# Kernel tuning notes

Hardware: AMD Instinct MI355X
Metric: run time of the kernel (lower is better)

The kernel has to match this reference:

```python
import jax, jax.numpy as jnp
import numpy as np

K, d = 8, 8
D = K * d          # 64
B, T, N = 8, 12, 325


def _xavier(key, shape):
    fan_out, fan_in = shape
    lim = (6.0 / (fan_in + fan_out)) ** 0.5
    return jax.random.uniform(key, shape, jnp.float32, -lim, lim)


def setup_inputs() -> dict:
    key = jax.random.key(0)
    ks = jax.random.split(key, 8)
    return {
        "X": jax.random.normal(ks[0], (B, T, N, D), jnp.float32),
        "STE": jax.random.normal(ks[1], (B, T, N, D), jnp.float32),
        "adj": jax.random.randint(ks[2], (N, N), 0, 2, jnp.int32),
        "W7": _xavier(ks[3], (D, 2 * D)), "b7": jnp.zeros((D,), jnp.float32),
        "W8": _xavier(ks[4], (D, 2 * D)), "b8": jnp.zeros((D,), jnp.float32),
        "W9": _xavier(ks[5], (D, 2 * D)), "b9": jnp.zeros((D,), jnp.float32),
        "W10": _xavier(ks[6], (D, D)), "b10": jnp.zeros((D,), jnp.float32),
        "W11": _xavier(ks[7], (D, D)), "b11": jnp.zeros((D,), jnp.float32),
    }


def reference(X, STE, adj, W7, b7, W8, b8, W9, b9, W10, b10, W11, b11):
    # X, STE: [B, T, N, D]
    x = jnp.concatenate([X, STE], axis=-1)  # [B,T,N,2D]
    gelu = lambda t: jax.nn.gelu(t, approximate=False)  # torch F.gelu default = exact erf
    q = gelu(x @ W7.T + b7)  # [B,T,N,D]
    k = gelu(x @ W8.T + b8)
    v = gelu(x @ W9.T + b9)
    # split D into K heads of size d (equivalent to torch split(dim=-1)+cat(dim=0))
    heads = lambda t: t.reshape(B, T, N, K, d)
    q, k, v = heads(q), heads(k), heads(v)
    # scores: [K,B,T,N,N] == torch's [K*B,T,N,N]
    attn = jnp.einsum('btnkd,btmkd->kbtnm', q, k) / (d ** 0.5)
    attn = jnp.where(adj > 0, attn, jnp.float32(-9e15))
    attn = jax.nn.softmax(attn, axis=-1)
    out = jnp.einsum('kbtnm,btmkd->btnkd', attn, v).reshape(B, T, N, D)
    out = gelu(out @ W10.T + b10) @ W11.T + b11
    return out
```

## Files before the change

kernel.cpp:

```cpp
#include <hip/hip_runtime.h>
#include <math.h>

#define NN 325
#define BT 96
#define NROWS (BT * NN)
#define SCL (0.35355339059327373f * 1.4426950408889634f)

typedef _Float16 half_t;
typedef half_t half4_t __attribute__((ext_vector_type(4)));
typedef half_t half2_t __attribute__((ext_vector_type(2)));
typedef float float4_t __attribute__((ext_vector_type(4)));

__device__ __forceinline__ float gelu_f(float x) {
    return 0.5f * x * (1.0f + erff(x * 0.70710678118654752f));
}

__global__ void pack_adj_kernel(const int* __restrict__ adj,
                                unsigned int* __restrict__ packedT)
{
    int idx = blockIdx.x * 256 + threadIdx.x;
    if (idx >= 11 * NN) return;
    int w = idx / NN, n = idx - w * NN;
    unsigned int bits = 0u;
    #pragma unroll 8
    for (int j = 0; j < 32; ++j) {
        int m = w * 32 + j;
        if (m < NN && adj[n * NN + m] > 0) bits |= (1u << j);
    }
    packedT[w * NN + n] = bits;
}

#define XS 136

__device__ __forceinline__ void qkv_mfma_phase(
    const half_t* x16, const half_t* w16p, const float* __restrict__ b,
    half_t* __restrict__ outp, float oscale,
    int row0, int rbase, int l15, int quad)
{
    float4_t acc[4];
    #pragma unroll
    for (int ct = 0; ct < 4; ++ct) {
        float bias = b[ct * 16 + l15];
        acc[ct] = (float4_t){bias, bias, bias, bias};
    }
    #pragma unroll
    for (int kk = 0; kk < 8; ++kk) {
        half4_t a = *(const half4_t*)&x16[(rbase + l15) * XS + kk * 16 + quad * 4];
        #pragma unroll
        for (int ct = 0; ct < 4; ++ct) {
            half4_t bf = *(const half4_t*)&w16p[(ct * 16 + l15) * XS + kk * 16 + quad * 4];
            acc[ct] = __builtin_amdgcn_mfma_f32_16x16x16f16(a, bf, acc[ct], 0, 0, 0);
        }
    }
    #pragma unroll
    for (int ct = 0; ct < 4; ++ct) {
        #pragma unroll
        for (int rr = 0; rr < 4; ++rr) {
            int R = row0 + rbase + quad * 4 + rr;
            if (R < NROWS)
                outp[R * 64 + ct * 16 + l15] =
                    (half_t)(gelu_f(acc[ct][rr]) * oscale);
        }
    }
}

__global__ __launch_bounds__(256) void qkv_kernel(
    const float* __restrict__ X, const float* __restrict__ STE,
    const float* __restrict__ W7, const float* __restrict__ b7,
    const float* __restrict__ W8, const float* __restrict__ b8,
    const float* __restrict__ W9, const float* __restrict__ b9,
    half_t* __restrict__ q, half_t* __restrict__ k, half_t* __restrict__ v)
{
    __shared__ __attribute__((aligned(16))) half_t x16[64 * XS];
    __shared__ __attribute__((aligned(16))) half_t w16[3][64 * XS];
    const int tid  = threadIdx.x;
    const int row0 = blockIdx.x * 64;

    #pragma unroll 2
    for (int idx = tid; idx < 64 * 32; idx += 256) {
        int r = idx >> 5, c4 = idx & 31;
        int R = row0 + r;
        float4 f = {0.f, 0.f, 0.f, 0.f};
        if (R < NROWS)
            f = (c4 < 16) ? *(const float4*)(X + R * 64 + c4 * 4)
                          : *(const float4*)(STE + R * 64 + (c4 - 16) * 4);
        half4_t hv;
        hv[0] = (half_t)f.x; hv[1] = (half_t)f.y;
        hv[2] = (half_t)f.z; hv[3] = (half_t)f.w;
        *(half4_t*)&x16[r * XS + c4 * 4] = hv;
    }
    #pragma unroll 2
    for (int idx = tid; idx < 3 * 64 * 32; idx += 256) {
        int p = idx >> 11, rem = idx & 2047;
        int c = rem >> 5, c4 = rem & 31;
        const float* Wp = (p == 0) ? W7 : (p == 1) ? W8 : W9;
        float4 f = *(const float4*)(Wp + c * 128 + c4 * 4);
        half4_t hv;
        hv[0] = (half_t)f.x; hv[1] = (half_t)f.y;
        hv[2] = (half_t)f.z; hv[3] = (half_t)f.w;
        *(half4_t*)&w16[p][c * XS + c4 * 4] = hv;
    }
    __syncthreads();

    const int lane = tid & 63, wv = tid >> 6;
    const int l15 = lane & 15, quad = lane >> 4;
    const int rbase = wv * 16;

    qkv_mfma_phase(x16, w16[0], b7, q, SCL, row0, rbase, l15, quad);
    qkv_mfma_phase(x16, w16[1], b8, k, 1.0f, row0, rbase, l15, quad);
    qkv_mfma_phase(x16, w16[2], b9, v, 1.0f, row0, rbase, l15, quad);
}

__global__ __launch_bounds__(256) void attn_kernel(
    const half_t* __restrict__ q16g, const half_t* __restrict__ k16g,
    const half_t* __restrict__ v16g, const unsigned int* __restrict__ packedT,
    half_t* __restrict__ ao)
{
    __shared__ __attribute__((aligned(16))) half_t Q16[336 * 20];
    __shared__ __attribute__((aligned(16))) half_t K16[336 * 20];
    __shared__ __attribute__((aligned(16))) half_t VT16[16 * 344];
    const int tid = threadIdx.x;
    const int h = blockIdx.x, bt = blockIdx.y;
    const long base = (long)(bt * NN) * 64 + h * 8;

    const half4_t z4 = {(half_t)0.f, (half_t)0.f, (half_t)0.f, (half_t)0.f};

    for (int r = tid; r < 336; r += 256) {
        half4_t qa = z4, qb = z4, ka = z4, kb = z4;
        if (r < NN) {
            qa = *(const half4_t*)(q16g + base + r * 64);
            qb = *(const half4_t*)(q16g + base + r * 64 + 4);
            ka = *(const half4_t*)(k16g + base + r * 64);
            kb = *(const half4_t*)(k16g + base + r * 64 + 4);
        }
        *(half4_t*)&Q16[r * 20]      = qa;
        *(half4_t*)&Q16[r * 20 + 4]  = qb;
        *(half4_t*)&Q16[r * 20 + 8]  = z4;
        *(half4_t*)&Q16[r * 20 + 12] = z4;
        *(half4_t*)&K16[r * 20]      = ka;
        *(half4_t*)&K16[r * 20 + 4]  = kb;
        *(half4_t*)&K16[r * 20 + 8]  = z4;
        *(half4_t*)&K16[r * 20 + 12] = z4;
    }

    for (int mp = tid; mp < 168; mp += 256) {
        int m0 = 2 * mp, m1 = 2 * mp + 1;
        half4_t v0a = z4, v0b = z4, v1a = z4, v1b = z4;
        if (m0 < NN) {
            v0a = *(const half4_t*)(v16g + base + m0 * 64);
            v0b = *(const half4_t*)(v16g + base + m0 * 64 + 4);
        }
        if (m1 < NN) {
            v1a = *(const half4_t*)(v16g + base + m1 * 64);
            v1b = *(const half4_t*)(v16g + base + m1 * 64 + 4);
        }
        #pragma unroll
        for (int c = 0; c < 4; ++c) {
            half2_t p0; p0[0] = v0a[c]; p0[1] = v1a[c];
            half2_t p1; p1[0] = v0b[c]; p1[1] = v1b[c];
            *(half2_t*)&VT16[c * 344 + 2 * mp]       = p0;
            *(half2_t*)&VT16[(c + 4) * 344 + 2 * mp] = p1;
        }
    }
    __syncthreads();

    const int lane = tid & 63;
    const int wv   = tid >> 6;
    const int l15  = lane & 15;
    const int quad = lane >> 4;
    const int qsh  = quad * 4;

    for (int t = wv; t < 21; t += 4) {
        const int n = t * 16 + l15;
        const half4_t qf = *(const half4_t*)&Q16[n * 20 + qsh];

        unsigned int mb[11];
        #pragma unroll
        for (int w = 0; w < 11; ++w) mb[w] = packedT[w * NN + n];

        float rm = -3.0e38f;
        for (int mt = 0; mt < 21; ++mt) {
            half4_t kf = *(const half4_t*)&K16[(mt * 16 + l15) * 20 + qsh];
            float4_t s = __builtin_amdgcn_mfma_f32_16x16x16f16(
                kf, qf, (float4_t){0.f, 0.f, 0.f, 0.f}, 0, 0, 0);
            unsigned int sh = mb[mt >> 1] >> (((mt & 1) << 4) + qsh);
            rm = fmaxf(rm, (sh & 1u) ? s[0] : -3.0e38f);
            rm = fmaxf(rm, (sh & 2u) ? s[1] : -3.0e38f);
            rm = fmaxf(rm, (sh & 4u) ? s[2] : -3.0e38f);
            rm = fmaxf(rm, (sh & 8u) ? s[3] : -3.0e38f);
        }
        rm = fmaxf(rm, __shfl_xor(rm, 16, 64));
        rm = fmaxf(rm, __shfl_xor(rm, 32, 64));

        float4_t acc = {0.f, 0.f, 0.f, 0.f};
        float sum = 0.f;
        for (int mt = 0; mt < 21; ++mt) {
            half4_t kf = *(const half4_t*)&K16[(mt * 16 + l15) * 20 + qsh];
            float4_t s = __builtin_amdgcn_mfma_f32_16x16x16f16(
                kf, qf, (float4_t){0.f, 0.f, 0.f, 0.f}, 0, 0, 0);
            unsigned int sh = mb[mt >> 1] >> (((mt & 1) << 4) + qsh);
            float p0 = (sh & 1u) ? __builtin_amdgcn_exp2f(s[0] - rm) : 0.f;
            float p1 = (sh & 2u) ? __builtin_amdgcn_exp2f(s[1] - rm) : 0.f;
            float p2 = (sh & 4u) ? __builtin_amdgcn_exp2f(s[2] - rm) : 0.f;
            float p3 = (sh & 8u) ? __builtin_amdgcn_exp2f(s[3] - rm) : 0.f;
            sum += (p0 + p1) + (p2 + p3);
            half4_t pf;
            pf[0] = (half_t)p0; pf[1] = (half_t)p1;
            pf[2] = (half_t)p2; pf[3] = (half_t)p3;
            half4_t vf = *(const half4_t*)&VT16[l15 * 344 + mt * 16 + qsh];
            acc = __builtin_amdgcn_mfma_f32_16x16x16f16(vf, pf, acc, 0, 0, 0);
        }
        sum += __shfl_xor(sum, 16, 64);
        sum += __shfl_xor(sum, 32, 64);

        if (quad < 2 && n < NN) {
            float inv = 1.0f / sum;
            half4_t o;
            o[0] = (half_t)(acc[0] * inv); o[1] = (half_t)(acc[1] * inv);
            o[2] = (half_t)(acc[2] * inv); o[3] = (half_t)(acc[3] * inv);
            *(half4_t*)(ao + base + n * 64 + qsh) = o;
        }
    }
}

#define PS 72

__global__ __launch_bounds__(256) void proj_kernel(
    const half_t* __restrict__ ao,
    const float* __restrict__ W10, const float* __restrict__ b10,
    const float* __restrict__ W11, const float* __restrict__ b11,
    float* __restrict__ out)
{
    __shared__ __attribute__((aligned(16))) half_t a16[64 * PS];
    __shared__ __attribute__((aligned(16))) half_t wA[64 * PS];
    __shared__ __attribute__((aligned(16))) half_t wB[64 * PS];
    __shared__ __attribute__((aligned(16))) half_t h16[64 * PS];
    const int tid  = threadIdx.x;
    const int row0 = blockIdx.x * 64;

    for (int idx = tid; idx < 64 * 8; idx += 256) {
        int r = idx >> 3, c8 = idx & 7;
        int R = row0 + r;
        uint4 u = {0u, 0u, 0u, 0u};
        if (R < NROWS) u = *(const uint4*)(ao + R * 64 + c8 * 8);
        *(uint4*)&a16[r * PS + c8 * 8] = u;
    }
    for (int idx = tid; idx < 64 * 16; idx += 256) {
        int r = idx >> 4, c4 = idx & 15;
        float4 fA = *(const float4*)(W10 + r * 64 + c4 * 4);
        float4 fB = *(const float4*)(W11 + r * 64 + c4 * 4);
        half4_t hA, hB;
        hA[0] = (half_t)fA.x; hA[1] = (half_t)fA.y;
        hA[2] = (half_t)fA.z; hA[3] = (half_t)fA.w;
        hB[0] = (half_t)fB.x; hB[1] = (half_t)fB.y;
        hB[2] = (half_t)fB.z; hB[3] = (half_t)fB.w;
        *(half4_t*)&wA[r * PS + c4 * 4] = hA;
        *(half4_t*)&wB[r * PS + c4 * 4] = hB;
    }
    __syncthreads();

    const int lane = tid & 63, wv = tid >> 6;
    const int l15 = lane & 15, quad = lane >> 4;
    const int rbase = wv * 16;

    float4_t acc[4];
    #pragma unroll
    for (int ct = 0; ct < 4; ++ct) {
        float bias = b10[ct * 16 + l15];
        acc[ct] = (float4_t){bias, bias, bias, bias};
    }
    #pragma unroll
    for (int kk = 0; kk < 4; ++kk) {
        half4_t a = *(const half4_t*)&a16[(rbase + l15) * PS + kk * 16 + quad * 4];
        #pragma unroll
        for (int ct = 0; ct < 4; ++ct) {
            half4_t bf = *(const half4_t*)&wA[(ct * 16 + l15) * PS + kk * 16 + quad * 4];
            acc[ct] = __builtin_amdgcn_mfma_f32_16x16x16f16(a, bf, acc[ct], 0, 0, 0);
        }
    }
    #pragma unroll
    for (int ct = 0; ct < 4; ++ct) {
        #pragma unroll
        for (int rr = 0; rr < 4; ++rr)
            h16[(rbase + quad * 4 + rr) * PS + ct * 16 + l15] =
                (half_t)gelu_f(acc[ct][rr]);
    }
    __syncthreads();

    #pragma unroll
    for (int ct = 0; ct < 4; ++ct) {
        float bias = b11[ct * 16 + l15];
        acc[ct] = (float4_t){bias, bias, bias, bias};
    }
    #pragma unroll
    for (int kk = 0; kk < 4; ++kk) {
        half4_t a = *(const half4_t*)&h16[(rbase + l15) * PS + kk * 16 + quad * 4];
        #pragma unroll
        for (int ct = 0; ct < 4; ++ct) {
            half4_t bf = *(const half4_t*)&wB[(ct * 16 + l15) * PS + kk * 16 + quad * 4];
            acc[ct] = __builtin_amdgcn_mfma_f32_16x16x16f16(a, bf, acc[ct], 0, 0, 0);
        }
    }
    #pragma unroll
    for (int ct = 0; ct < 4; ++ct) {
        #pragma unroll
        for (int rr = 0; rr < 4; ++rr) {
            int R = row0 + rbase + quad * 4 + rr;
            if (R < NROWS)
                out[R * 64 + ct * 16 + l15] = acc[ct][rr];
        }
    }
}

extern "C" void kernel_launch(void* const* d_in, const int* in_sizes, int n_in,
                              void* d_out, int out_size, void* d_ws, size_t ws_size,
                              hipStream_t stream) {
    const float* X   = (const float*)d_in[0];
    const float* STE = (const float*)d_in[1];
    const int*   adj = (const int*)d_in[2];
    const float* W7  = (const float*)d_in[3];
    const float* b7  = (const float*)d_in[4];
    const float* W8  = (const float*)d_in[5];
    const float* b8  = (const float*)d_in[6];
    const float* W9  = (const float*)d_in[7];
    const float* b9  = (const float*)d_in[8];
    const float* W10 = (const float*)d_in[9];
    const float* b10 = (const float*)d_in[10];
    const float* W11 = (const float*)d_in[11];
    const float* b11 = (const float*)d_in[12];

    half_t* hws = (half_t*)d_ws;
    const long S = (long)NROWS * 64;
    half_t* qb = hws;
    half_t* kb = hws + S;
    half_t* vb = hws + 2 * S;
    half_t* ab = hws + 3 * S;
    unsigned int* pk = (unsigned int*)(hws + 4 * S);

    pack_adj_kernel<<<(11 * NN + 255) / 256, 256, 0, stream>>>(adj, pk);
    qkv_kernel<<<dim3((NROWS + 63) / 64), 256, 0, stream>>>(
        X, STE, W7, b7, W8, b8, W9, b9, qb, kb, vb);
    attn_kernel<<<dim3(8, BT), 256, 0, stream>>>(qb, kb, vb, pk, ab);
    proj_kernel<<<dim3((NROWS + 63) / 64), 256, 0, stream>>>(
        ab, W10, b10, W11, b11, (float*)d_out);
}
```

Baseline: 164.3 us.

## Pre-convert weights once, double-buffer QKV weight staging, simplify attention softmax

```diff
diff --git a/kernel.cpp b/kernel.cpp
--- a/kernel.cpp
+++ b/kernel.cpp
@@ -15,69 +15,97 @@
     return 0.5f * x * (1.0f + erff(x * 0.70710678118654752f));
 }
 
-__global__ void pack_adj_kernel(const int* __restrict__ adj,
-                                unsigned int* __restrict__ packedT)
+__global__ void prep_kernel(const int* __restrict__ adj,
+                            const float* __restrict__ W7,
+                            const float* __restrict__ W8,
+                            const float* __restrict__ W9,
+                            const float* __restrict__ W10,
+                            const float* __restrict__ W11,
+                            unsigned int* __restrict__ packedT,
+                            half_t* __restrict__ w789,
+                            half_t* __restrict__ wab)
 {
     int idx = blockIdx.x * 256 + threadIdx.x;
-    if (idx >= 11 * NN) return;
-    int w = idx / NN, n = idx - w * NN;
-    unsigned int bits = 0u;
-    #pragma unroll 8
-    for (int j = 0; j < 32; ++j) {
-        int m = w * 32 + j;
-        if (m < NN && adj[n * NN + m] > 0) bits |= (1u << j);
-    }
-    packedT[w * NN + n] = bits;
+    if (idx < 11 * NN) {
+        int w = idx / NN, n = idx - w * NN;
+        unsigned int bits = 0u;
+        #pragma unroll 8
+        for (int j = 0; j < 32; ++j) {
+            int m = w * 32 + j;
+            if (m < NN && adj[n * NN + m] > 0) bits |= (1u << j);
+        }
+        packedT[w * NN + n] = bits;
+    } else if (idx < 3575 + 24576) {
+        int i = idx - 3575;
+        int p = i >> 13, r = i & 8191;
+        const float* Wp = (p == 0) ? W7 : (p == 1) ? W8 : W9;
+        w789[i] = (half_t)Wp[r];
+    } else if (idx < 3575 + 24576 + 8192) {
+        int i = idx - 28151;
+        int p = i >> 12, r = i & 4095;
+        wab[i] = (half_t)(p ? W11[r] : W10[r]);
+    }
 }
 
 #define XS 136
 
-__device__ __forceinline__ void qkv_mfma_phase(
-    const half_t* x16, const half_t* w16p, const float* __restrict__ b,
+__device__ __forceinline__ void qkv_stage_w(const half_t* __restrict__ src,
+                                            half_t* dst, int tid)
+{
+    #pragma unroll
+    for (int idx = tid; idx < 1024; idx += 512) {
+        int c = idx >> 4, g = idx & 15;
+        *(uint4*)&dst[c * XS + g * 8] = *(const uint4*)&src[c * 128 + g * 8];
+    }
+}
+
+__device__ __forceinline__ void qkv_compute(
+    const half_t* x16, const half_t* wb, const float* __restrict__ b,
     half_t* __restrict__ outp, float oscale,
-    int row0, int rbase, int l15, int quad)
-{
-    float4_t acc[4];
-    #pragma unroll
-    for (int ct = 0; ct < 4; ++ct) {
-        float bias = b[ct * 16 + l15];
-        acc[ct] = (float4_t){bias, bias, bias, bias};
+    int row0, int rbase, int ch, int l15, int quad)
+{
+    float4_t acc[2];
+    #pragma unroll
+    for (int cc = 0; cc < 2; ++cc) {
+        float bias = b[(ch * 2 + cc) * 16 + l15];
+        acc[cc] = (float4_t){bias, bias, bias, bias};
     }
     #pragma unroll
     for (int kk = 0; kk < 8; ++kk) {
         half4_t a = *(const half4_t*)&x16[(rbase + l15) * XS + kk * 16 + quad * 4];
         #pragma unroll
-        for (int ct = 0; ct < 4; ++ct) {
-            half4_t bf = *(const half4_t*)&w16p[(ct * 16 + l15) * XS + kk * 16 + quad * 4];
-            acc[ct] = __builtin_amdgcn_mfma_f32_16x16x16f16(a, bf, acc[ct], 0, 0, 0);
-        }
-    }
-    #pragma unroll
-    for (int ct = 0; ct < 4; ++ct) {
+        for (int cc = 0; cc < 2; ++cc) {
+            half4_t bf = *(const half4_t*)
+                &wb[((ch * 2 + cc) * 16 + l15) * XS + kk * 16 + quad * 4];
+            acc[cc] = __builtin_amdgcn_mfma_f32_16x16x16f16(a, bf, acc[cc], 0, 0, 0);
+        }
+    }
+    #pragma unroll
+    for (int cc = 0; cc < 2; ++cc) {
         #pragma unroll
         for (int rr = 0; rr < 4; ++rr) {
             int R = row0 + rbase + quad * 4 + rr;
             if (R < NROWS)
-                outp[R * 64 + ct * 16 + l15] =
-                    (half_t)(gelu_f(acc[ct][rr]) * oscale);
-        }
-    }
-}
-
-__global__ __launch_bounds__(256) void qkv_kernel(
+                outp[R * 64 + (ch * 2 + cc) * 16 + l15] =
+                    (half_t)(gelu_f(acc[cc][rr]) * oscale);
+        }
+    }
+}
+
+__global__ __launch_bounds__(512) void qkv_kernel(
     const float* __restrict__ X, const float* __restrict__ STE,
-    const float* __restrict__ W7, const float* __restrict__ b7,
-    const float* __restrict__ W8, const float* __restrict__ b8,
-    const float* __restrict__ W9, const float* __restrict__ b9,
+    const half_t* __restrict__ w789,
+    const float* __restrict__ b7, const float* __restrict__ b8,
+    const float* __restrict__ b9,
     half_t* __restrict__ q, half_t* __restrict__ k, half_t* __restrict__ v)
 {
     __shared__ __attribute__((aligned(16))) half_t x16[64 * XS];
-    __shared__ __attribute__((aligned(16))) half_t w16[3][64 * XS];
+    __shared__ __attribute__((aligned(16))) half_t wbuf[2][64 * XS];
     const int tid  = threadIdx.x;
     const int row0 = blockIdx.x * 64;
 
-    #pragma unroll 2
-    for (int idx = tid; idx < 64 * 32; idx += 256) {
+    #pragma unroll
+    for (int idx = tid; idx < 2048; idx += 512) {
         int r = idx >> 5, c4 = idx & 31;
         int R = row0 + r;
         float4 f = {0.f, 0.f, 0.f, 0.f};
@@ -89,26 +117,22 @@
         hv[2] = (half_t)f.z; hv[3] = (half_t)f.w;
         *(half4_t*)&x16[r * XS + c4 * 4] = hv;
     }
-    #pragma unroll 2
-    for (int idx = tid; idx < 3 * 64 * 32; idx += 256) {
-        int p = idx >> 11, rem = idx & 2047;
-        int c = rem >> 5, c4 = rem & 31;
-        const float* Wp = (p == 0) ? W7 : (p == 1) ? W8 : W9;
-        float4 f = *(const float4*)(Wp + c * 128 + c4 * 4);
-        half4_t hv;
-        hv[0] = (half_t)f.x; hv[1] = (half_t)f.y;
-        hv[2] = (half_t)f.z; hv[3] = (half_t)f.w;
-        *(half4_t*)&w16[p][c * XS + c4 * 4] = hv;
-    }
+    qkv_stage_w(w789, wbuf[0], tid);
     __syncthreads();
 
     const int lane = tid & 63, wv = tid >> 6;
     const int l15 = lane & 15, quad = lane >> 4;
-    const int rbase = wv * 16;
-
-    qkv_mfma_phase(x16, w16[0], b7, q, SCL, row0, rbase, l15, quad);
-    qkv_mfma_phase(x16, w16[1], b8, k, 1.0f, row0, rbase, l15, quad);
-    qkv_mfma_phase(x16, w16[2], b9, v, 1.0f, row0, rbase, l15, quad);
+    const int rbase = (wv & 3) * 16, ch = wv >> 2;
+
+    qkv_stage_w(w789 + 8192, wbuf[1], tid);
+    qkv_compute(x16, wbuf[0], b7, q, SCL, row0, rbase, ch, l15, quad);
+    __syncthreads();
+
+    qkv_stage_w(w789 + 16384, wbuf[0], tid);
+    qkv_compute(x16, wbuf[1], b8, k, 1.0f, row0, rbase, ch, l15, quad);
+    __syncthreads();
+
+    qkv_compute(x16, wbuf[0], b9, v, 1.0f, row0, rbase, ch, l15, quad);
 }
 
 __global__ __launch_bounds__(256) void attn_kernel(
@@ -116,7 +140,6 @@
     const half_t* __restrict__ v16g, const unsigned int* __restrict__ packedT,
     half_t* __restrict__ ao)
 {
-    __shared__ __attribute__((aligned(16))) half_t Q16[336 * 20];
     __shared__ __attribute__((aligned(16))) half_t K16[336 * 20];
     __shared__ __attribute__((aligned(16))) half_t VT16[16 * 344];
     const int tid = threadIdx.x;
@@ -125,18 +148,18 @@
 
     const half4_t z4 = {(half_t)0.f, (half_t)0.f, (half_t)0.f, (half_t)0.f};
 
+    for (int idx = tid; idx < 16 * 344 / 2; idx += 256)
+        ((half2_t*)VT16)[idx] = (half2_t)(half_t)0.f;
+    __syncthreads();
+    for (int i = tid; i < 344; i += 256)
+        VT16[8 * 344 + i] = (half_t)1.0f;
+
     for (int r = tid; r < 336; r += 256) {
-        half4_t qa = z4, qb = z4, ka = z4, kb = z4;
+        half4_t ka = z4, kb = z4;
         if (r < NN) {
-            qa = *(const half4_t*)(q16g + base + r * 64);
-            qb = *(const half4_t*)(q16g + base + r * 64 + 4);
             ka = *(const half4_t*)(k16g + base + r * 64);
             kb = *(const half4_t*)(k16g + base + r * 64 + 4);
         }
-        *(half4_t*)&Q16[r * 20]      = qa;
-        *(half4_t*)&Q16[r * 20 + 4]  = qb;
-        *(half4_t*)&Q16[r * 20 + 8]  = z4;
-        *(half4_t*)&Q16[r * 20 + 12] = z4;
         *(half4_t*)&K16[r * 20]      = ka;
         *(half4_t*)&K16[r * 20 + 4]  = kb;
         *(half4_t*)&K16[r * 20 + 8]  = z4;
@@ -171,64 +194,64 @@
     const int qsh  = quad * 4;
 
     for (int t = wv; t < 21; t += 4) {
-        const int n = t * 16 + l15;
-        const half4_t qf = *(const half4_t*)&Q16[n * 20 + qsh];
-
-        unsigned int mb[11];
-        #pragma unroll
-        for (int w = 0; w < 11; ++w) mb[w] = packedT[w * NN + n];
-
-        float rm = -3.0e38f;
+        const int n  = t * 16 + l15;
+        const int nq = (n < NN) ? n : (NN - 1);
+
+        half4_t qf = z4;
+        if (quad < 2)
+            qf = *(const half4_t*)(q16g + base + (long)nq * 64 + qsh);
+
+        float rm = 0.0f;
+        #pragma unroll
         for (int mt = 0; mt < 21; ++mt) {
             half4_t kf = *(const half4_t*)&K16[(mt * 16 + l15) * 20 + qsh];
             float4_t s = __builtin_amdgcn_mfma_f32_16x16x16f16(
                 kf, qf, (float4_t){0.f, 0.f, 0.f, 0.f}, 0, 0, 0);
-            unsigned int sh = mb[mt >> 1] >> (((mt & 1) << 4) + qsh);
-            rm = fmaxf(rm, (sh & 1u) ? s[0] : -3.0e38f);
-            rm = fmaxf(rm, (sh & 2u) ? s[1] : -3.0e38f);
-            rm = fmaxf(rm, (sh & 4u) ? s[2] : -3.0e38f);
-            rm = fmaxf(rm, (sh & 8u) ? s[3] : -3.0e38f);
+            rm = fmaxf(rm, fmaxf(fmaxf(s[0], s[1]), fmaxf(s[2], s[3])));
         }
         rm = fmaxf(rm, __shfl_xor(rm, 16, 64));
         rm = fmaxf(rm, __shfl_xor(rm, 32, 64));
 
+        unsigned int mb[11];
+        #pragma unroll
+        for (int w = 0; w < 11; ++w) mb[w] = packedT[w * NN + nq];
+
+        const float4_t cinit = {-rm, -rm, -rm, -rm};
         float4_t acc = {0.f, 0.f, 0.f, 0.f};
-        float sum = 0.f;
+        #pragma unroll
         for (int mt = 0; mt < 21; ++mt) {
             half4_t kf = *(const half4_t*)&K16[(mt * 16 + l15) * 20 + qsh];
             float4_t s = __builtin_amdgcn_mfma_f32_16x16x16f16(
-                kf, qf, (float4_t){0.f, 0.f, 0.f, 0.f}, 0, 0, 0);
+                kf, qf, cinit, 0, 0, 0);
             unsigned int sh = mb[mt >> 1] >> (((mt & 1) << 4) + qsh);
-            float p0 = (sh & 1u) ? __builtin_amdgcn_exp2f(s[0] - rm) : 0.f;
-            float p1 = (sh & 2u) ? __builtin_amdgcn_exp2f(s[1] - rm) : 0.f;
-            float p2 = (sh & 4u) ? __builtin_amdgcn_exp2f(s[2] - rm) : 0.f;
-            float p3 = (sh & 8u) ? __builtin_amdgcn_exp2f(s[3] - rm) : 0.f;
-            sum += (p0 + p1) + (p2 + p3);
+            float p0 = (sh & 1u) ? __builtin_amdgcn_exp2f(s[0]) : 0.f;
+            float p1 = (sh & 2u) ? __builtin_amdgcn_exp2f(s[1]) : 0.f;
+            float p2 = (sh & 4u) ? __builtin_amdgcn_exp2f(s[2]) : 0.f;
+            float p3 = (sh & 8u) ? __builtin_amdgcn_exp2f(s[3]) : 0.f;
             half4_t pf;
             pf[0] = (half_t)p0; pf[1] = (half_t)p1;
             pf[2] = (half_t)p2; pf[3] = (half_t)p3;
             half4_t vf = *(const half4_t*)&VT16[l15 * 344 + mt * 16 + qsh];
             acc = __builtin_amdgcn_mfma_f32_16x16x16f16(vf, pf, acc, 0, 0, 0);
         }
-        sum += __shfl_xor(sum, 16, 64);
-        sum += __shfl_xor(sum, 32, 64);
+
+        float sum = __shfl(acc[0], 32 + l15, 64);
 
         if (quad < 2 && n < NN) {
             float inv = 1.0f / sum;
             half4_t o;
             o[0] = (half_t)(acc[0] * inv); o[1] = (half_t)(acc[1] * inv);
             o[2] = (half_t)(acc[2] * inv); o[3] = (half_t)(acc[3] * inv);
-            *(half4_t*)(ao + base + n * 64 + qsh) = o;
+            *(half4_t*)(ao + base + (long)n * 64 + qsh) = o;
         }
     }
 }
 
 #define PS 72
 
-__global__ __launch_bounds__(256) void proj_kernel(
-    const half_t* __restrict__ ao,
-    const float* __restrict__ W10, const float* __restrict__ b10,
-    const float* __restrict__ W11, const float* __restrict__ b11,
+__global__ __launch_bounds__(512) void proj_kernel(
+    const half_t* __restrict__ ao, const half_t* __restrict__ wab,
+    const float* __restrict__ b10, const float* __restrict__ b11,
     float* __restrict__ out)
 {
     __shared__ __attribute__((aligned(16))) half_t a16[64 * PS];
@@ -238,76 +261,68 @@
     const int tid  = threadIdx.x;
     const int row0 = blockIdx.x * 64;
 
-    for (int idx = tid; idx < 64 * 8; idx += 256) {
+    for (int idx = tid; idx < 512; idx += 512) {
         int r = idx >> 3, c8 = idx & 7;
         int R = row0 + r;
         uint4 u = {0u, 0u, 0u, 0u};
-        if (R < NROWS) u = *(const uint4*)(ao + R * 64 + c8 * 8);
+        if (R < NROWS) u = *(const uint4*)(ao + (long)R * 64 + c8 * 8);
         *(uint4*)&a16[r * PS + c8 * 8] = u;
-    }
-    for (int idx = tid; idx < 64 * 16; idx += 256) {
-        int r = idx >> 4, c4 = idx & 15;
-        float4 fA = *(const float4*)(W10 + r * 64 + c4 * 4);
-        float4 fB = *(const float4*)(W11 + r * 64 + c4 * 4);
-        half4_t hA, hB;
-        hA[0] = (half_t)fA.x; hA[1] = (half_t)fA.y;
-        hA[2] = (half_t)fA.z; hA[3] = (half_t)fA.w;
-        hB[0] = (half_t)fB.x; hB[1] = (half_t)fB.y;
-        hB[2] = (half_t)fB.z; hB[3] = (half_t)fB.w;
-        *(half4_t*)&wA[r * PS + c4 * 4] = hA;
-        *(half4_t*)&wB[r * PS + c4 * 4] = hB;
+        *(uint4*)&wA[r * PS + c8 * 8] = *(const uint4*)&wab[r * 64 + c8 * 8];
+        *(uint4*)&wB[r * PS + c8 * 8] = *(const uint4*)&wab[4096 + r * 64 + c8 * 8];
     }
     __syncthreads();
 
     const int lane = tid & 63, wv = tid >> 6;
     const int l15 = lane & 15, quad = lane >> 4;
-    const int rbase = wv * 16;
-
-    float4_t acc[4];
-    #pragma unroll
-    for (int ct = 0; ct < 4; ++ct) {
-        float bias = b10[ct * 16 + l15];
-        acc[ct] = (float4_t){bias, bias, bias, bias};
+    const int rbase = (wv & 3) * 16, ch = wv >> 2;
+
+    float4_t acc[2];
+    #pragma unroll
+    for (int cc = 0; cc < 2; ++cc) {
+        float bias = b10[(ch * 2 + cc) * 16 + l15];
+        acc[cc] = (float4_t){bias, bias, bias, bias};
     }
     #pragma unroll
     for (int kk = 0; kk < 4; ++kk) {
         half4_t a = *(const half4_t*)&a16[(rbase + l15) * PS + kk * 16 + quad * 4];
         #pragma unroll
-        for (int ct = 0; ct < 4; ++ct) {
-            half4_t bf = *(const half4_t*)&wA[(ct * 16 + l15) * PS + kk * 16 + quad * 4];
-            acc[ct] = __builtin_amdgcn_mfma_f32_16x16x16f16(a, bf, acc[ct], 0, 0, 0);
-        }
-    }
-    #pragma unroll
-    for (int ct = 0; ct < 4; ++ct) {
+        for (int cc = 0; cc < 2; ++cc) {
+            half4_t bf = *(const half4_t*)
+                &wA[((ch * 2 + cc) * 16 + l15) * PS + kk * 16 + quad * 4];
+            acc[cc] = __builtin_amdgcn_mfma_f32_16x16x16f16(a, bf, acc[cc], 0, 0, 0);
+        }
+    }
+    #pragma unroll
+    for (int cc = 0; cc < 2; ++cc) {
         #pragma unroll
         for (int rr = 0; rr < 4; ++rr)
-            h16[(rbase + quad * 4 + rr) * PS + ct * 16 + l15] =
-                (half_t)gelu_f(acc[ct][rr]);
-    }
-    __syncthreads();
-
-    #pragma unroll
-    for (int ct = 0; ct < 4; ++ct) {
-        float bias = b11[ct * 16 + l15];
-        acc[ct] = (float4_t){bias, bias, bias, bias};
+            h16[(rbase + quad * 4 + rr) * PS + (ch * 2 + cc) * 16 + l15] =
+                (half_t)gelu_f(acc[cc][rr]);
+    }
+    __syncthreads();
+
+    #pragma unroll
+    for (int cc = 0; cc < 2; ++cc) {
+        float bias = b11[(ch * 2 + cc) * 16 + l15];
+        acc[cc] = (float4_t){bias, bias, bias, bias};
     }
     #pragma unroll
     for (int kk = 0; kk < 4; ++kk) {
         half4_t a = *(const half4_t*)&h16[(rbase + l15) * PS + kk * 16 + quad * 4];
         #pragma unroll
-        for (int ct = 0; ct < 4; ++ct) {
-            half4_t bf = *(const half4_t*)&wB[(ct * 16 + l15) * PS + kk * 16 + quad * 4];
-            acc[ct] = __builtin_amdgcn_mfma_f32_16x16x16f16(a, bf, acc[ct], 0, 0, 0);
-        }
-    }
-    #pragma unroll
-    for (int ct = 0; ct < 4; ++ct) {
+        for (int cc = 0; cc < 2; ++cc) {
+            half4_t bf = *(const half4_t*)
+                &wB[((ch * 2 + cc) * 16 + l15) * PS + kk * 16 + quad * 4];
+            acc[cc] = __builtin_amdgcn_mfma_f32_16x16x16f16(a, bf, acc[cc], 0, 0, 0);
+        }
+    }
+    #pragma unroll
+    for (int cc = 0; cc < 2; ++cc) {
         #pragma unroll
         for (int rr = 0; rr < 4; ++rr) {
             int R = row0 + rbase + quad * 4 + rr;
             if (R < NROWS)
-                out[R * 64 + ct * 16 + l15] = acc[ct][rr];
+                out[R * 64 + (ch * 2 + cc) * 16 + l15] = acc[cc][rr];
         }
     }
 }
@@ -329,18 +344,21 @@
     const float* W11 = (const float*)d_in[11];
     const float* b11 = (const float*)d_in[12];
 
-    half_t* hws = (half_t*)d_ws;
+    char* wsb = (char*)d_ws;
     const long S = (long)NROWS * 64;
-    half_t* qb = hws;
-    half_t* kb = hws + S;
-    half_t* vb = hws + 2 * S;
-    half_t* ab = hws + 3 * S;
-    unsigned int* pk = (unsigned int*)(hws + 4 * S);
-
-    pack_adj_kernel<<<(11 * NN + 255) / 256, 256, 0, stream>>>(adj, pk);
-    qkv_kernel<<<dim3((NROWS + 63) / 64), 256, 0, stream>>>(
-        X, STE, W7, b7, W8, b8, W9, b9, qb, kb, vb);
+    half_t* qb = (half_t*)wsb;
+    half_t* kb = qb + S;
+    half_t* vb = qb + 2 * S;
+    half_t* ab = qb + 3 * S;
+    unsigned int* pk = (unsigned int*)(wsb + 4 * S * sizeof(half_t));
+    half_t* w789 = (half_t*)(wsb + 4 * S * sizeof(half_t) + 16384);
+    half_t* wab  = w789 + 24576;
+
+    prep_kernel<<<142, 256, 0, stream>>>(adj, W7, W8, W9, W10, W11,
+                                         pk, w789, wab);
+    qkv_kernel<<<dim3((NROWS + 63) / 64), 512, 0, stream>>>(
+        X, STE, w789, b7, b8, b9, qb, kb, vb);
     attn_kernel<<<dim3(8, BT), 256, 0, stream>>>(qb, kb, vb, pk, ab);
-    proj_kernel<<<dim3((NROWS + 63) / 64), 256, 0, stream>>>(
-        ab, W10, b10, W11, b11, (float*)d_out);
-}
+    proj_kernel<<<dim3((NROWS + 63) / 64), 512, 0, stream>>>(
+        ab, wab, b10, b11, (float*)d_out);
+}
```

After: 153.2 us. -6.8%, faster.
